# Optimization experiments

Hardware: AMD Instinct MI355X
Metric: run time of the kernel (lower is better)

Reference implementation:

```python
import jax, jax.numpy as jnp
import numpy as np

TOP_K = 2
AUX_COEF = 1e-3

def setup_inputs() -> dict:
    key = jax.random.key(0)
    ks = jax.random.split(key, 5)
    B, S, H, I, E = 4, 2048, 1024, 2048, 8
    x = jax.random.normal(ks[0], (B, S, H), jnp.float32)
    gate_w = jax.random.normal(ks[1], (H, E), jnp.float32) * 0.02
    w_gate = jax.random.normal(ks[2], (E, H, I), jnp.float32) * 0.02
    w_up = jax.random.normal(ks[3], (E, H, I), jnp.float32) * 0.02
    w_down = jax.random.normal(ks[4], (E, I, H), jnp.float32) * 0.02
    return {"x": x, "gate_w": gate_w, "w_gate": w_gate, "w_up": w_up, "w_down": w_down}


def reference(x, gate_w, w_gate, w_up, w_down):
    B, S, H = x.shape
    E = gate_w.shape[1]
    xf = x.reshape(-1, H)              # [N, H]
    N = xf.shape[0]

    # Router: softmax in fp32 (matches F.softmax(..., dtype=torch.float32))
    logits = xf @ gate_w               # [N, E]
    rw = jax.nn.softmax(logits.astype(jnp.float32), axis=-1).astype(x.dtype)
    top_w, top_i = jax.lax.top_k(rw, TOP_K)            # [N, K]
    top_w = top_w / top_w.sum(axis=-1, keepdims=True)  # renormalize

    # Combine weights: comb[t, e] = sum_k top_w[t,k] * (top_i[t,k]==e)
    comb = jnp.zeros((N, E), x.dtype).at[jnp.arange(N)[:, None], top_i].add(top_w)

    # SwiGLU FFN computed densely per expert, masked/combined by router weights
    h_gate = jax.nn.silu(jnp.einsum('th,ehi->eti', xf, w_gate))   # [E, N, I]
    h_up = jnp.einsum('th,ehi->eti', xf, w_up)                    # [E, N, I]
    expert_out = jnp.einsum('eti,eih->eth', h_gate * h_up, w_down)  # [E, N, H]
    y = jnp.einsum('eth,te->th', expert_out, comb).reshape(B, S, H)

    # Load-balancing aux loss
    sel_w = jnp.take_along_axis(rw, top_i, axis=1)   # router weight of chosen experts [N, K]
    load = jnp.zeros((E,), rw.dtype).at[top_i.reshape(-1)].add(sel_w.reshape(-1))
    P_expert = load / N
    counts = jnp.zeros((E,), jnp.float32).at[top_i.reshape(-1)].add(1.0)
    P_token_expert = counts / (N * TOP_K)
    aux_loss = (P_expert * P_token_expert).sum() * E * AUX_COEF
    return y, aux_loss
```

## Files before the change

kernel.cpp:

```cpp
#include <hip/hip_runtime.h>

#define N_TOK 8192
#define H_DIM 1024
#define I_DIM 2048
#define N_EXP 8
#define TOPK  2
#define CAP   17408
#define MT_MAX 136

#define OFF_TOPK_I 0u
#define OFF_TOPK_W 65536u
#define OFF_COUNTS 131072u
#define OFF_LOAD   131104u
#define OFF_CURSOR 131136u
#define OFF_PO     131168u
#define OFF_TILE_E 131232u
#define OFF_BTOK   131840u
#define OFF_BW     201472u
#define CTRL_BYTES 271104u
#define OFF_TSLOT  271104u
#define OFF_WGT  1048576u
#define OFF_WUT  (OFF_WGT + 33554432u)
#define OFF_WDT  (OFF_WUT + 33554432u)
#define OFF_HB   (OFF_WDT + 33554432u)
#define OFF_XB   (OFF_HB + 71303168u)

typedef __attribute__((ext_vector_type(8))) short bf16x8;
typedef __attribute__((ext_vector_type(8))) unsigned short u16x8;
typedef __attribute__((ext_vector_type(4))) unsigned short u16x4;
typedef __attribute__((ext_vector_type(4))) float f32x4;

__device__ __forceinline__ unsigned short f2bf(float f) {
  union { float f; unsigned int u; } v; v.f = f;
  unsigned int r = (v.u + 0x7FFFu + ((v.u >> 16) & 1u)) >> 16;
  return (unsigned short)r;
}
__device__ __forceinline__ float bf2f(unsigned short u) {
  union { unsigned int u; float f; } v; v.u = ((unsigned int)u) << 16;
  return v.f;
}
__device__ __forceinline__ u16x8 pack8(float4 a, float4 b) {
  u16x8 r;
  r[0] = f2bf(a.x); r[1] = f2bf(a.y); r[2] = f2bf(a.z); r[3] = f2bf(a.w);
  r[4] = f2bf(b.x); r[5] = f2bf(b.y); r[6] = f2bf(b.z); r[7] = f2bf(b.w);
  return r;
}
__device__ __forceinline__ f32x4 mfma32(bf16x8 a, bf16x8 b, f32x4 c) {
  return __builtin_amdgcn_mfma_f32_16x16x32_bf16(a, b, c, 0, 0, 0);
}
__device__ __forceinline__ void gll16(const void* g, void* l) {
  __builtin_amdgcn_global_load_lds(
      (const __attribute__((address_space(1))) unsigned int*)g,
      (__attribute__((address_space(3))) unsigned int*)l, 16, 0, 0);
}

__global__ __launch_bounds__(256) void k_xcast(const float* __restrict__ x,
                                               unsigned short* __restrict__ xb)
{
  int idx = blockIdx.x * 256 + threadIdx.x;
  const float4* s = (const float4*)x + (size_t)idx * 2;
  float4 a = s[0], b = s[1];
  *(u16x8*)&xb[(size_t)idx * 8] = pack8(a, b);
}

__global__ __launch_bounds__(256) void k_transpose(
    const float* __restrict__ wg, const float* __restrict__ wu, const float* __restrict__ wd,
    unsigned short* __restrict__ wgT, unsigned short* __restrict__ wuT,
    unsigned short* __restrict__ wdT)
{
  __shared__ unsigned short lds[64][65];
  int bid = blockIdx.x;
  int m = bid / 4096; int rem = bid % 4096;
  const float* src; unsigned short* dst; int R, C;
  if (m == 0)      { src = wg; dst = wgT; R = 1024; C = 2048; }
  else if (m == 1) { src = wu; dst = wuT; R = 1024; C = 2048; }
  else             { src = wd; dst = wdT; R = 2048; C = 1024; }
  int e = rem / 512; int trem = rem % 512;
  int tcc = C / 64;
  int r0 = (trem / tcc) * 64, c0 = (trem % tcc) * 64;
  size_t ebase = (size_t)e * R * C;
  dst += ebase;
  int tid = threadIdx.x;
  int lr = tid >> 3;
  int lc = (tid & 7) * 8;
#pragma unroll
  for (int p = 0; p < 2; ++p) {
    int row = p * 32 + lr;
    size_t off = ebase + (size_t)(r0 + row) * C + c0 + lc;
    float4 q0 = *(const float4*)&src[off];
    float4 q1 = *(const float4*)&src[off + 4];
    unsigned short tmp[8]; *(u16x8*)tmp = pack8(q0, q1);
#pragma unroll
    for (int j = 0; j < 8; ++j) lds[row][lc + j] = tmp[j];
  }
  __syncthreads();
#pragma unroll
  for (int p = 0; p < 2; ++p) {
    int drow = p * 32 + lr;
    unsigned short tmp[8];
#pragma unroll
    for (int j = 0; j < 8; ++j) tmp[j] = lds[lc + j][drow];
    *(u16x8*)&dst[(size_t)(c0 + drow) * R + r0 + lc] = *(const u16x8*)tmp;
  }
}

__global__ __launch_bounds__(256) void k_router(
    const float* __restrict__ x, const float* __restrict__ gw,
    int* __restrict__ topk_i, float* __restrict__ topk_w)
{
  int wave = threadIdx.x >> 6, lane = threadIdx.x & 63;
  int t = blockIdx.x * 4 + wave;
  const float* xr = x + (size_t)t * H_DIM;
  float acc[8];
#pragma unroll
  for (int e = 0; e < 8; ++e) acc[e] = 0.f;
#pragma unroll
  for (int it = 0; it < H_DIM / 64; ++it) {
    int h = it * 64 + lane;
    float xv = xr[h];
    float4 g0 = *(const float4*)&gw[h * 8];
    float4 g1 = *(const float4*)&gw[h * 8 + 4];
    acc[0] += xv * g0.x; acc[1] += xv * g0.y; acc[2] += xv * g0.z; acc[3] += xv * g0.w;
    acc[4] += xv * g1.x; acc[5] += xv * g1.y; acc[6] += xv * g1.z; acc[7] += xv * g1.w;
  }
#pragma unroll
  for (int off = 32; off > 0; off >>= 1) {
#pragma unroll
    for (int e = 0; e < 8; ++e) acc[e] += __shfl_xor(acc[e], off);
  }
  if (lane == 0) {
    float m = acc[0];
#pragma unroll
    for (int e = 1; e < 8; ++e) m = fmaxf(m, acc[e]);
    float p[8], s = 0.f;
#pragma unroll
    for (int e = 0; e < 8; ++e) { p[e] = __expf(acc[e] - m); s += p[e]; }
    float inv = 1.f / s;
#pragma unroll
    for (int e = 0; e < 8; ++e) p[e] *= inv;
    int i1 = 0;
#pragma unroll
    for (int e = 1; e < 8; ++e) if (p[e] > p[i1]) i1 = e;
    int i2 = (i1 == 0) ? 1 : 0;
#pragma unroll
    for (int e = 0; e < 8; ++e) if (e != i1 && p[e] > p[i2]) i2 = e;
    topk_i[t * 2]     = i1; topk_i[t * 2 + 1] = i2;
    topk_w[t * 2]     = p[i1]; topk_w[t * 2 + 1] = p[i2];
  }
}

__global__ __launch_bounds__(256) void k_hist(
    const int* __restrict__ topk_i, const float* __restrict__ topk_w,
    int* __restrict__ counts, float* __restrict__ loadw)
{
  __shared__ int c[8]; __shared__ float l[8];
  int tid = threadIdx.x;
  if (tid < 8) { c[tid] = 0; l[tid] = 0.f; }
  __syncthreads();
  int base = blockIdx.x * 1024 + tid * 4;
#pragma unroll
  for (int j = 0; j < 4; ++j) {
    int e = topk_i[base + j];
    float w = topk_w[base + j];
    atomicAdd(&c[e], 1);
    atomicAdd(&l[e], w);
  }
  __syncthreads();
  if (tid < 8) { atomicAdd(&counts[tid], c[tid]); atomicAdd(&loadw[tid], l[tid]); }
}

__global__ __launch_bounds__(256) void k_offsets(
    const int* __restrict__ counts, const float* __restrict__ loadw,
    int* __restrict__ po, int* __restrict__ tile_e, float* __restrict__ out)
{
  __shared__ int spo[9];
  if (threadIdx.x == 0) {
    int a = 0;
    for (int e = 0; e < 8; ++e) { spo[e] = a; po[e] = a; a += (counts[e] + 127) & ~127; }
    spo[8] = a; po[8] = a;
    float s = 0.f;
    for (int e = 0; e < 8; ++e) s += loadw[e] * (float)counts[e];
    out[(size_t)N_TOK * H_DIM] =
        s * ((float)N_EXP * 1e-3f) / ((float)N_TOK * (float)N_TOK * (float)TOPK);
  }
  __syncthreads();
  int mt = threadIdx.x;
  if (mt < MT_MAX) {
    int te = -1, beg = mt * 128;
    if (beg < spo[8]) {
      for (int e = 0; e < 8; ++e) if (beg >= spo[e] && beg < spo[e + 1]) te = e;
    }
    tile_e[mt] = te;
  }
}

__global__ __launch_bounds__(256) void k_bucket(
    const int* __restrict__ topk_i, const float* __restrict__ topk_w,
    const int* __restrict__ po, int* __restrict__ cursor,
    int* __restrict__ btok, float* __restrict__ bw, int* __restrict__ tslot)
{
  __shared__ int c[8];
  __shared__ int basee[8];
  int tid = threadIdx.x;
  if (tid < 8) c[tid] = 0;
  __syncthreads();
  int base = blockIdx.x * 1024 + tid * 4;
  int e4[4], r4[4]; float w4[4];
#pragma unroll
  for (int j = 0; j < 4; ++j) {
    int idx = base + j;
    int e = topk_i[idx];
    e4[j] = e;
    r4[j] = atomicAdd(&c[e], 1);
    int t = idx >> 1;
    float p0 = topk_w[t * 2], p1 = topk_w[t * 2 + 1];
    w4[j] = topk_w[idx] / (p0 + p1);
  }
  __syncthreads();
  if (tid < 8) basee[tid] = po[tid] + atomicAdd(&cursor[tid], c[tid]);
  __syncthreads();
#pragma unroll
  for (int j = 0; j < 4; ++j) {
    int idx = base + j;
    int slot = basee[e4[j]] + r4[j];
    btok[slot] = idx >> 1;
    bw[slot] = w4[j];
    tslot[idx] = slot;
  }
}

__global__ __launch_bounds__(256, 2) void k_gemm1(
    const unsigned short* __restrict__ xb,
    const unsigned short* __restrict__ wgT, const unsigned short* __restrict__ wuT,
    const int* __restrict__ btok, const int* __restrict__ tile_e,
    unsigned short* __restrict__ hbuf)
{
  int mt = blockIdx.y, nt = blockIdx.x;
  int e = tile_e[mt];
  if (e < 0) return;
  __shared__ unsigned short As[128 * 32];
  __shared__ unsigned short Bg[128 * 32];
  __shared__ unsigned short Bu[128 * 32];
  int tid = threadIdx.x;
  int wave = tid >> 6, lane = tid & 63;
  int wm = wave >> 1, wn = wave & 1;
  int quad = lane >> 4, l16 = lane & 15;

  int srow = lane >> 2;
  int sko  = (lane & 3) * 8;
  int ar0 = wave * 16 + srow;
  int ar1 = 64 + wave * 16 + srow;
  int t0 = btok[mt * 128 + ar0];
  int t1 = btok[mt * 128 + ar1];
  const unsigned short* ga0 = xb + (size_t)t0 * H_DIM + sko;
  const unsigned short* ga1 = xb + (size_t)t1 * H_DIM + sko;
  const unsigned short* bgb = wgT + ((size_t)e * I_DIM + nt * 128) * H_DIM;
  const unsigned short* bub = wuT + ((size_t)e * I_DIM + nt * 128) * H_DIM;
  const unsigned short* gg0 = bgb + (size_t)ar0 * H_DIM + sko;
  const unsigned short* gg1 = bgb + (size_t)ar1 * H_DIM + sko;
  const unsigned short* gu0 = bub + (size_t)ar0 * H_DIM + sko;
  const unsigned short* gu1 = bub + (size_t)ar1 * H_DIM + sko;
  unsigned lb0 = (unsigned)(wave * 16) * 32;
  unsigned lb1 = (unsigned)(64 + wave * 16) * 32;

  f32x4 accG[4][4], accU[4][4];
  f32x4 z = {0.f, 0.f, 0.f, 0.f};
#pragma unroll
  for (int i = 0; i < 4; ++i)
#pragma unroll
    for (int j = 0; j < 4; ++j) { accG[i][j] = z; accU[i][j] = z; }

  for (int k0 = 0; k0 < H_DIM; k0 += 32) {
    gll16(ga0 + k0, &As[lb0]);
    gll16(ga1 + k0, &As[lb1]);
    gll16(gg0 + k0, &Bg[lb0]);
    gll16(gg1 + k0, &Bg[lb1]);
    gll16(gu0 + k0, &Bu[lb0]);
    gll16(gu1 + k0, &Bu[lb1]);
    __syncthreads();
    bf16x8 af[4];
#pragma unroll
    for (int i = 0; i < 4; ++i)
      af[i] = *(const bf16x8*)&As[(wm * 64 + i * 16 + l16) * 32 + quad * 8];
#pragma unroll
    for (int j = 0; j < 4; ++j) {
      bf16x8 vg = *(const bf16x8*)&Bg[(wn * 64 + j * 16 + l16) * 32 + quad * 8];
      bf16x8 vu = *(const bf16x8*)&Bu[(wn * 64 + j * 16 + l16) * 32 + quad * 8];
#pragma unroll
      for (int i = 0; i < 4; ++i) {
        accG[i][j] = mfma32(af[i], vg, accG[i][j]);
        accU[i][j] = mfma32(af[i], vu, accU[i][j]);
      }
    }
    __syncthreads();
  }
#pragma unroll
  for (int i = 0; i < 4; ++i) {
#pragma unroll
    for (int r = 0; r < 4; ++r) {
      int row = mt * 128 + wm * 64 + i * 16 + quad * 4 + r;
      size_t base = (size_t)row * I_DIM + nt * 128 + wn * 64 + l16;
#pragma unroll
      for (int j = 0; j < 4; ++j) {
        float g = accG[i][j][r], u = accU[i][j][r];
        float sg = g / (1.f + __expf(-g));
        hbuf[base + j * 16] = f2bf(sg * u);
      }
    }
  }
}

__global__ __launch_bounds__(256, 2) void k_gemm2(
    const unsigned short* __restrict__ hbuf, const unsigned short* __restrict__ wdT,
    const int* __restrict__ tile_e, unsigned short* __restrict__ obuf)
{
  int mt = blockIdx.y, nt = blockIdx.x;
  int e = tile_e[mt];
  if (e < 0) return;
  __shared__ unsigned short As[128 * 32];
  __shared__ unsigned short Bs[128 * 32];
  int tid = threadIdx.x;
  int wave = tid >> 6, lane = tid & 63;
  int wm = wave >> 1, wn = wave & 1;
  int quad = lane >> 4, l16 = lane & 15;

  int srow = lane >> 2;
  int sko  = (lane & 3) * 8;
  int ar0 = wave * 16 + srow;
  int ar1 = 64 + wave * 16 + srow;
  const unsigned short* ga0 = hbuf + (size_t)(mt * 128 + ar0) * I_DIM + sko;
  const unsigned short* ga1 = hbuf + (size_t)(mt * 128 + ar1) * I_DIM + sko;
  const unsigned short* bb = wdT + ((size_t)e * H_DIM + nt * 128) * I_DIM;
  const unsigned short* gb0 = bb + (size_t)ar0 * I_DIM + sko;
  const unsigned short* gb1 = bb + (size_t)ar1 * I_DIM + sko;
  unsigned lb0 = (unsigned)(wave * 16) * 32;
  unsigned lb1 = (unsigned)(64 + wave * 16) * 32;

  f32x4 acc[4][4];
  f32x4 z = {0.f, 0.f, 0.f, 0.f};
#pragma unroll
  for (int i = 0; i < 4; ++i)
#pragma unroll
    for (int j = 0; j < 4; ++j) acc[i][j] = z;

  for (int k0 = 0; k0 < I_DIM; k0 += 32) {
    gll16(ga0 + k0, &As[lb0]);
    gll16(ga1 + k0, &As[lb1]);
    gll16(gb0 + k0, &Bs[lb0]);
    gll16(gb1 + k0, &Bs[lb1]);
    __syncthreads();
    bf16x8 af[4];
#pragma unroll
    for (int i = 0; i < 4; ++i)
      af[i] = *(const bf16x8*)&As[(wm * 64 + i * 16 + l16) * 32 + quad * 8];
#pragma unroll
    for (int j = 0; j < 4; ++j) {
      bf16x8 vb = *(const bf16x8*)&Bs[(wn * 64 + j * 16 + l16) * 32 + quad * 8];
#pragma unroll
      for (int i = 0; i < 4; ++i) acc[i][j] = mfma32(af[i], vb, acc[i][j]);
    }
    __syncthreads();
  }
#pragma unroll
  for (int i = 0; i < 4; ++i) {
#pragma unroll
    for (int r = 0; r < 4; ++r) {
      int s = mt * 128 + wm * 64 + i * 16 + quad * 4 + r;
      size_t base = (size_t)s * H_DIM + nt * 128 + wn * 64 + l16;
#pragma unroll
      for (int j = 0; j < 4; ++j)
        obuf[base + j * 16] = f2bf(acc[i][j][r]);
    }
  }
}

__global__ __launch_bounds__(256) void k_final(
    const unsigned short* __restrict__ obuf, const int* __restrict__ tslot,
    const float* __restrict__ bw, float* __restrict__ y)
{
  int t = blockIdx.x;
  int s0 = tslot[t * 2], s1 = tslot[t * 2 + 1];
  float w0 = bw[s0], w1 = bw[s1];
  int c = threadIdx.x * 4;
  u16x4 o0 = *(const u16x4*)&obuf[(size_t)s0 * H_DIM + c];
  u16x4 o1 = *(const u16x4*)&obuf[(size_t)s1 * H_DIM + c];
  float4 r;
  r.x = w0 * bf2f(o0[0]) + w1 * bf2f(o1[0]);
  r.y = w0 * bf2f(o0[1]) + w1 * bf2f(o1[1]);
  r.z = w0 * bf2f(o0[2]) + w1 * bf2f(o1[2]);
  r.w = w0 * bf2f(o0[3]) + w1 * bf2f(o1[3]);
  *(float4*)&y[(size_t)t * H_DIM + c] = r;
}

extern "C" void kernel_launch(void* const* d_in, const int* in_sizes, int n_in,
                              void* d_out, int out_size, void* d_ws, size_t ws_size,
                              hipStream_t stream)
{
  (void)in_sizes; (void)n_in; (void)out_size; (void)ws_size;
  const float* x  = (const float*)d_in[0];
  const float* gw = (const float*)d_in[1];
  const float* wg = (const float*)d_in[2];
  const float* wu = (const float*)d_in[3];
  const float* wd = (const float*)d_in[4];
  char* ws = (char*)d_ws;

  int*   topk_i = (int*)  (ws + OFF_TOPK_I);
  float* topk_w = (float*)(ws + OFF_TOPK_W);
  int*   counts = (int*)  (ws + OFF_COUNTS);
  float* loadw  = (float*)(ws + OFF_LOAD);
  int*   cursor = (int*)  (ws + OFF_CURSOR);
  int*   po     = (int*)  (ws + OFF_PO);
  int*   tile_e = (int*)  (ws + OFF_TILE_E);
  int*   btok   = (int*)  (ws + OFF_BTOK);
  float* bw     = (float*)(ws + OFF_BW);
  int*   tslot  = (int*)  (ws + OFF_TSLOT);
  unsigned short* wgT  = (unsigned short*)(ws + OFF_WGT);
  unsigned short* wuT  = (unsigned short*)(ws + OFF_WUT);
  unsigned short* wdT  = (unsigned short*)(ws + OFF_WDT);
  unsigned short* hbuf = (unsigned short*)(ws + OFF_HB);
  unsigned short* xb   = (unsigned short*)(ws + OFF_XB);
  unsigned short* obuf = (unsigned short*)(ws + OFF_WGT);
  float* yout = (float*)d_out;

  (void)hipMemsetAsync(ws, 0, CTRL_BYTES, stream);
  k_xcast<<<(N_TOK * H_DIM) / 2048, 256, 0, stream>>>(x, xb);
  k_transpose<<<12288, 256, 0, stream>>>(wg, wu, wd, wgT, wuT, wdT);
  k_router<<<N_TOK / 4, 256, 0, stream>>>(x, gw, topk_i, topk_w);
  k_hist<<<16, 256, 0, stream>>>(topk_i, topk_w, counts, loadw);
  k_offsets<<<1, 256, 0, stream>>>(counts, loadw, po, tile_e, (float*)d_out);
  k_bucket<<<16, 256, 0, stream>>>(topk_i, topk_w, po, cursor, btok, bw, tslot);
  k_gemm1<<<dim3(I_DIM / 128, MT_MAX), 256, 0, stream>>>(xb, wgT, wuT, btok, tile_e, hbuf);
  k_gemm2<<<dim3(H_DIM / 128, MT_MAX), 256, 0, stream>>>(hbuf, wdT, tile_e, obuf);
  k_final<<<N_TOK, 256, 0, stream>>>(obuf, tslot, bw, yout);
}
```

Before: 575.9 us.

## Rewrite expert GEMMs with 256-row tiles, swizzled LDS, multi-buffered prefetch pipelines

Both grouped GEMM kernels move to 512-thread blocks with 256-row M tiles, and expert buckets are padded to multiples of 256. The LDS layout uses a 64-wide K slab with an XOR swizzle to avoid bank conflicts. Global-to-LDS loads are prefetched into double buffers in gemm1 and triple buffers in gemm2, interleaved with MFMA phases using s_setprio and explicit vmcnt waits. The aim is to raise data reuse and hide memory latency, at the cost of more padding waste per expert and higher LDS use that limits occupancy.

```diff
diff --git a/kernel.cpp b/kernel.cpp
--- a/kernel.cpp
+++ b/kernel.cpp
@@ -5,8 +5,8 @@
 #define I_DIM 2048
 #define N_EXP 8
 #define TOPK  2
-#define CAP   17408
-#define MT_MAX 136
+#define CAP   18432
+#define MT_MAX 72
 
 #define OFF_TOPK_I 0u
 #define OFF_TOPK_W 65536u
@@ -15,20 +15,26 @@
 #define OFF_CURSOR 131136u
 #define OFF_PO     131168u
 #define OFF_TILE_E 131232u
-#define OFF_BTOK   131840u
-#define OFF_BW     201472u
-#define CTRL_BYTES 271104u
-#define OFF_TSLOT  271104u
+#define OFF_BTOK   131744u
+#define OFF_BW     205472u
+#define CTRL_BYTES 279200u
+#define OFF_TSLOT  279552u
 #define OFF_WGT  1048576u
 #define OFF_WUT  (OFF_WGT + 33554432u)
 #define OFF_WDT  (OFF_WUT + 33554432u)
 #define OFF_HB   (OFF_WDT + 33554432u)
-#define OFF_XB   (OFF_HB + 71303168u)
+#define OFF_XB   (OFF_HB + 75497472u)
 
 typedef __attribute__((ext_vector_type(8))) short bf16x8;
 typedef __attribute__((ext_vector_type(8))) unsigned short u16x8;
 typedef __attribute__((ext_vector_type(4))) unsigned short u16x4;
 typedef __attribute__((ext_vector_type(4))) float f32x4;
+
+#define BAR() __builtin_amdgcn_s_barrier()
+#define PRIO1() __builtin_amdgcn_s_setprio(1)
+#define PRIO0() __builtin_amdgcn_s_setprio(0)
+#define WAITV0() asm volatile("s_waitcnt vmcnt(0)" ::: "memory")
+#define WAITV6() asm volatile("s_waitcnt vmcnt(6)" ::: "memory")
 
 __device__ __forceinline__ unsigned short f2bf(float f) {
   union { float f; unsigned int u; } v; v.f = f;
@@ -176,7 +182,7 @@
   __shared__ int spo[9];
   if (threadIdx.x == 0) {
     int a = 0;
-    for (int e = 0; e < 8; ++e) { spo[e] = a; po[e] = a; a += (counts[e] + 127) & ~127; }
+    for (int e = 0; e < 8; ++e) { spo[e] = a; po[e] = a; a += (counts[e] + 255) & ~255; }
     spo[8] = a; po[8] = a;
     float s = 0.f;
     for (int e = 0; e < 8; ++e) s += loadw[e] * (float)counts[e];
@@ -186,7 +192,7 @@
   __syncthreads();
   int mt = threadIdx.x;
   if (mt < MT_MAX) {
-    int te = -1, beg = mt * 128;
+    int te = -1, beg = mt * 256;
     if (beg < spo[8]) {
       for (int e = 0; e < 8; ++e) if (beg >= spo[e] && beg < spo[e + 1]) te = e;
     }
@@ -229,7 +235,7 @@
   }
 }
 
-__global__ __launch_bounds__(256, 2) void k_gemm1(
+__global__ __launch_bounds__(512, 2) void k_gemm1(
     const unsigned short* __restrict__ xb,
     const unsigned short* __restrict__ wgT, const unsigned short* __restrict__ wuT,
     const int* __restrict__ btok, const int* __restrict__ tile_e,
@@ -238,30 +244,32 @@
   int mt = blockIdx.y, nt = blockIdx.x;
   int e = tile_e[mt];
   if (e < 0) return;
-  __shared__ unsigned short As[128 * 32];
-  __shared__ unsigned short Bg[128 * 32];
-  __shared__ unsigned short Bu[128 * 32];
+  __shared__ unsigned short lds[65536];
   int tid = threadIdx.x;
   int wave = tid >> 6, lane = tid & 63;
   int wm = wave >> 1, wn = wave & 1;
   int quad = lane >> 4, l16 = lane & 15;
 
-  int srow = lane >> 2;
-  int sko  = (lane & 3) * 8;
-  int ar0 = wave * 16 + srow;
-  int ar1 = 64 + wave * 16 + srow;
-  int t0 = btok[mt * 128 + ar0];
-  int t1 = btok[mt * 128 + ar1];
-  const unsigned short* ga0 = xb + (size_t)t0 * H_DIM + sko;
-  const unsigned short* ga1 = xb + (size_t)t1 * H_DIM + sko;
-  const unsigned short* bgb = wgT + ((size_t)e * I_DIM + nt * 128) * H_DIM;
-  const unsigned short* bub = wuT + ((size_t)e * I_DIM + nt * 128) * H_DIM;
-  const unsigned short* gg0 = bgb + (size_t)ar0 * H_DIM + sko;
-  const unsigned short* gg1 = bgb + (size_t)ar1 * H_DIM + sko;
-  const unsigned short* gu0 = bub + (size_t)ar0 * H_DIM + sko;
-  const unsigned short* gu1 = bub + (size_t)ar1 * H_DIM + sko;
-  unsigned lb0 = (unsigned)(wave * 16) * 32;
-  unsigned lb1 = (unsigned)(64 + wave * 16) * 32;
+  int rp = lane >> 3;
+  int chunk = (lane & 7) ^ rp;
+  const unsigned short* sA[2][2]; const unsigned short* sBg[2]; const unsigned short* sBu[2];
+  unsigned dA[2][2], dB[2];
+#pragma unroll
+  for (int h = 0; h < 2; ++h)
+#pragma unroll
+    for (int c = 0; c < 2; ++c) {
+      int rowp = wave * 16 + c * 8 + rp;
+      int tok = btok[mt * 256 + h * 128 + rowp];
+      sA[h][c] = xb + (size_t)tok * H_DIM + chunk * 8;
+      dA[h][c] = (unsigned)(h * 128 + wave * 16 + c * 8) * 64;
+    }
+#pragma unroll
+  for (int c = 0; c < 2; ++c) {
+    int rowp = wave * 16 + c * 8 + rp;
+    sBg[c] = wgT + ((size_t)e * I_DIM + nt * 128 + rowp) * H_DIM + chunk * 8;
+    sBu[c] = wuT + ((size_t)e * I_DIM + nt * 128 + rowp) * H_DIM + chunk * 8;
+    dB[c] = (unsigned)(wave * 16 + c * 8) * 64;
+  }
 
   f32x4 accG[4][4], accU[4][4];
   f32x4 z = {0.f, 0.f, 0.f, 0.f};
@@ -270,108 +278,251 @@
 #pragma unroll
     for (int j = 0; j < 4; ++j) { accG[i][j] = z; accU[i][j] = z; }
 
-  for (int k0 = 0; k0 < H_DIM; k0 += 32) {
-    gll16(ga0 + k0, &As[lb0]);
-    gll16(ga1 + k0, &As[lb1]);
-    gll16(gg0 + k0, &Bg[lb0]);
-    gll16(gg1 + k0, &Bg[lb1]);
-    gll16(gu0 + k0, &Bu[lb0]);
-    gll16(gu1 + k0, &Bu[lb1]);
-    __syncthreads();
-    bf16x8 af[4];
-#pragma unroll
-    for (int i = 0; i < 4; ++i)
-      af[i] = *(const bf16x8*)&As[(wm * 64 + i * 16 + l16) * 32 + quad * 8];
-#pragma unroll
-    for (int j = 0; j < 4; ++j) {
-      bf16x8 vg = *(const bf16x8*)&Bg[(wn * 64 + j * 16 + l16) * 32 + quad * 8];
-      bf16x8 vu = *(const bf16x8*)&Bu[(wn * 64 + j * 16 + l16) * 32 + quad * 8];
-#pragma unroll
-      for (int i = 0; i < 4; ++i) {
-        accG[i][j] = mfma32(af[i], vg, accG[i][j]);
-        accU[i][j] = mfma32(af[i], vu, accU[i][j]);
-      }
-    }
-    __syncthreads();
-  }
-#pragma unroll
-  for (int i = 0; i < 4; ++i) {
+  int fsw = l16 & 7;
+#pragma unroll
+  for (int h = 0; h < 2; ++h)
+#pragma unroll
+    for (int c = 0; c < 2; ++c) gll16(sA[h][c], &lds[dA[h][c]]);
+#pragma unroll
+  for (int c = 0; c < 2; ++c) { gll16(sBg[c], &lds[16384 + dB[c]]); gll16(sBu[c], &lds[24576 + dB[c]]); }
+  WAITV0();
+  BAR();
+
+  for (int t = 0; t < 16; ++t) {
+    unsigned bo = (unsigned)(t & 1) * 32768;
+    unsigned bo1 = bo ^ 32768;
+    int kel = (t + 1) * 64;
+    bool pf = (t < 15);
+    bf16x8 a[4][2];
+#pragma unroll
+    for (int m = 0; m < 4; ++m)
+#pragma unroll
+      for (int ks = 0; ks < 2; ++ks) {
+        int row = wm * 64 + m * 16 + l16;
+        a[m][ks] = *(const bf16x8*)&lds[bo + row * 64 + (((ks * 4 + quad) ^ fsw) * 8)];
+      }
+    bf16x8 bg[2][2];
+#pragma unroll
+    for (int nf = 0; nf < 2; ++nf)
+#pragma unroll
+      for (int ks = 0; ks < 2; ++ks) {
+        int col = wn * 64 + nf * 16 + l16;
+        bg[nf][ks] = *(const bf16x8*)&lds[bo + 16384 + col * 64 + (((ks * 4 + quad) ^ fsw) * 8)];
+      }
+    if (pf) {
+#pragma unroll
+      for (int h = 0; h < 2; ++h)
+#pragma unroll
+        for (int c = 0; c < 2; ++c) gll16(sA[h][c] + kel, &lds[bo1 + dA[h][c]]);
+    }
+    BAR();
+    PRIO1();
+#pragma unroll
+    for (int nf = 0; nf < 2; ++nf)
+#pragma unroll
+      for (int m = 0; m < 4; ++m)
+#pragma unroll
+        for (int ks = 0; ks < 2; ++ks) accG[m][nf] = mfma32(a[m][ks], bg[nf][ks], accG[m][nf]);
+    PRIO0();
+    BAR();
+#pragma unroll
+    for (int nf = 0; nf < 2; ++nf)
+#pragma unroll
+      for (int ks = 0; ks < 2; ++ks) {
+        int col = wn * 64 + (2 + nf) * 16 + l16;
+        bg[nf][ks] = *(const bf16x8*)&lds[bo + 16384 + col * 64 + (((ks * 4 + quad) ^ fsw) * 8)];
+      }
+    if (pf) {
+#pragma unroll
+      for (int c = 0; c < 2; ++c) { gll16(sBg[c] + kel, &lds[bo1 + 16384 + dB[c]]); gll16(sBu[c] + kel, &lds[bo1 + 24576 + dB[c]]); }
+    }
+    BAR();
+    PRIO1();
+#pragma unroll
+    for (int nf = 0; nf < 2; ++nf)
+#pragma unroll
+      for (int m = 0; m < 4; ++m)
+#pragma unroll
+        for (int ks = 0; ks < 2; ++ks) accG[m][2 + nf] = mfma32(a[m][ks], bg[nf][ks], accG[m][2 + nf]);
+    PRIO0();
+    BAR();
+#pragma unroll
+    for (int nf = 0; nf < 2; ++nf)
+#pragma unroll
+      for (int ks = 0; ks < 2; ++ks) {
+        int col = wn * 64 + nf * 16 + l16;
+        bg[nf][ks] = *(const bf16x8*)&lds[bo + 24576 + col * 64 + (((ks * 4 + quad) ^ fsw) * 8)];
+      }
+    BAR();
+    PRIO1();
+#pragma unroll
+    for (int nf = 0; nf < 2; ++nf)
+#pragma unroll
+      for (int m = 0; m < 4; ++m)
+#pragma unroll
+        for (int ks = 0; ks < 2; ++ks) accU[m][nf] = mfma32(a[m][ks], bg[nf][ks], accU[m][nf]);
+    PRIO0();
+    BAR();
+#pragma unroll
+    for (int nf = 0; nf < 2; ++nf)
+#pragma unroll
+      for (int ks = 0; ks < 2; ++ks) {
+        int col = wn * 64 + (2 + nf) * 16 + l16;
+        bg[nf][ks] = *(const bf16x8*)&lds[bo + 24576 + col * 64 + (((ks * 4 + quad) ^ fsw) * 8)];
+      }
+    BAR();
+    PRIO1();
+#pragma unroll
+    for (int nf = 0; nf < 2; ++nf)
+#pragma unroll
+      for (int m = 0; m < 4; ++m)
+#pragma unroll
+        for (int ks = 0; ks < 2; ++ks) accU[m][2 + nf] = mfma32(a[m][ks], bg[nf][ks], accU[m][2 + nf]);
+    PRIO0();
+    WAITV0();
+    BAR();
+  }
+#pragma unroll
+  for (int m = 0; m < 4; ++m)
 #pragma unroll
     for (int r = 0; r < 4; ++r) {
-      int row = mt * 128 + wm * 64 + i * 16 + quad * 4 + r;
+      int row = mt * 256 + wm * 64 + m * 16 + quad * 4 + r;
       size_t base = (size_t)row * I_DIM + nt * 128 + wn * 64 + l16;
 #pragma unroll
-      for (int j = 0; j < 4; ++j) {
-        float g = accG[i][j][r], u = accU[i][j][r];
+      for (int nf = 0; nf < 4; ++nf) {
+        float g = accG[m][nf][r], u = accU[m][nf][r];
         float sg = g / (1.f + __expf(-g));
-        hbuf[base + j * 16] = f2bf(sg * u);
-      }
-    }
-  }
-}
-
-__global__ __launch_bounds__(256, 2) void k_gemm2(
+        hbuf[base + nf * 16] = f2bf(sg * u);
+      }
+    }
+}
+
+__global__ __launch_bounds__(512, 2) void k_gemm2(
     const unsigned short* __restrict__ hbuf, const unsigned short* __restrict__ wdT,
     const int* __restrict__ tile_e, unsigned short* __restrict__ obuf)
 {
   int mt = blockIdx.y, nt = blockIdx.x;
   int e = tile_e[mt];
   if (e < 0) return;
-  __shared__ unsigned short As[128 * 32];
-  __shared__ unsigned short Bs[128 * 32];
+  __shared__ unsigned short lds[73728];
   int tid = threadIdx.x;
   int wave = tid >> 6, lane = tid & 63;
-  int wm = wave >> 1, wn = wave & 1;
+  int wm = wave >> 2, wn = wave & 3;
   int quad = lane >> 4, l16 = lane & 15;
 
-  int srow = lane >> 2;
-  int sko  = (lane & 3) * 8;
-  int ar0 = wave * 16 + srow;
-  int ar1 = 64 + wave * 16 + srow;
-  const unsigned short* ga0 = hbuf + (size_t)(mt * 128 + ar0) * I_DIM + sko;
-  const unsigned short* ga1 = hbuf + (size_t)(mt * 128 + ar1) * I_DIM + sko;
-  const unsigned short* bb = wdT + ((size_t)e * H_DIM + nt * 128) * I_DIM;
-  const unsigned short* gb0 = bb + (size_t)ar0 * I_DIM + sko;
-  const unsigned short* gb1 = bb + (size_t)ar1 * I_DIM + sko;
-  unsigned lb0 = (unsigned)(wave * 16) * 32;
-  unsigned lb1 = (unsigned)(64 + wave * 16) * 32;
-
-  f32x4 acc[4][4];
+  int rp = lane >> 3;
+  int chunk = (lane & 7) ^ rp;
+  const unsigned short* sA[2][2]; const unsigned short* sB[2];
+  unsigned dA[2][2], dB[2];
+#pragma unroll
+  for (int h = 0; h < 2; ++h)
+#pragma unroll
+    for (int c = 0; c < 2; ++c) {
+      int rowp = wave * 16 + c * 8 + rp;
+      sA[h][c] = hbuf + (size_t)(mt * 256 + h * 128 + rowp) * I_DIM + chunk * 8;
+      dA[h][c] = (unsigned)(h * 128 + wave * 16 + c * 8) * 64;
+    }
+#pragma unroll
+  for (int c = 0; c < 2; ++c) {
+    int rowp = wave * 16 + c * 8 + rp;
+    sB[c] = wdT + ((size_t)e * H_DIM + nt * 128 + rowp) * I_DIM + chunk * 8;
+    dB[c] = (unsigned)(wave * 16 + c * 8) * 64;
+  }
+
+  f32x4 acc[8][2];
   f32x4 z = {0.f, 0.f, 0.f, 0.f};
 #pragma unroll
-  for (int i = 0; i < 4; ++i)
-#pragma unroll
-    for (int j = 0; j < 4; ++j) acc[i][j] = z;
-
-  for (int k0 = 0; k0 < I_DIM; k0 += 32) {
-    gll16(ga0 + k0, &As[lb0]);
-    gll16(ga1 + k0, &As[lb1]);
-    gll16(gb0 + k0, &Bs[lb0]);
-    gll16(gb1 + k0, &Bs[lb1]);
-    __syncthreads();
-    bf16x8 af[4];
-#pragma unroll
-    for (int i = 0; i < 4; ++i)
-      af[i] = *(const bf16x8*)&As[(wm * 64 + i * 16 + l16) * 32 + quad * 8];
-#pragma unroll
-    for (int j = 0; j < 4; ++j) {
-      bf16x8 vb = *(const bf16x8*)&Bs[(wn * 64 + j * 16 + l16) * 32 + quad * 8];
-#pragma unroll
-      for (int i = 0; i < 4; ++i) acc[i][j] = mfma32(af[i], vb, acc[i][j]);
-    }
-    __syncthreads();
-  }
-#pragma unroll
-  for (int i = 0; i < 4; ++i) {
+  for (int i = 0; i < 8; ++i) { acc[i][0] = z; acc[i][1] = z; }
+
+  int fsw = l16 & 7;
+#pragma unroll
+  for (int tt = 0; tt < 2; ++tt) {
+    unsigned bo = (unsigned)tt * 24576;
+    int kel = tt * 64;
+#pragma unroll
+    for (int h = 0; h < 2; ++h)
+#pragma unroll
+      for (int c = 0; c < 2; ++c) gll16(sA[h][c] + kel, &lds[bo + dA[h][c]]);
+#pragma unroll
+    for (int c = 0; c < 2; ++c) gll16(sB[c] + kel, &lds[bo + 16384 + dB[c]]);
+  }
+  WAITV6();
+  BAR();
+
+  unsigned boA = 0, boB = 24576, boC = 49152;
+  for (int t = 0; t < 32; ++t) {
+    int kel = (t + 2) * 64;
+    bool pf = (t < 30);
+    bf16x8 b[2][2];
+#pragma unroll
+    for (int nf = 0; nf < 2; ++nf)
+#pragma unroll
+      for (int ks = 0; ks < 2; ++ks) {
+        int col = wn * 32 + nf * 16 + l16;
+        b[nf][ks] = *(const bf16x8*)&lds[boA + 16384 + col * 64 + (((ks * 4 + quad) ^ fsw) * 8)];
+      }
+    {
+      bf16x8 a[4][2];
+#pragma unroll
+      for (int m = 0; m < 4; ++m)
+#pragma unroll
+        for (int ks = 0; ks < 2; ++ks) {
+          int row = wm * 128 + m * 16 + l16;
+          a[m][ks] = *(const bf16x8*)&lds[boA + row * 64 + (((ks * 4 + quad) ^ fsw) * 8)];
+        }
+      if (pf) {
+#pragma unroll
+        for (int h = 0; h < 2; ++h)
+#pragma unroll
+          for (int c = 0; c < 2; ++c) gll16(sA[h][c] + kel, &lds[boC + dA[h][c]]);
+      }
+      BAR();
+      PRIO1();
+#pragma unroll
+      for (int m = 0; m < 4; ++m)
+#pragma unroll
+        for (int nf = 0; nf < 2; ++nf)
+#pragma unroll
+          for (int ks = 0; ks < 2; ++ks) acc[m][nf] = mfma32(a[m][ks], b[nf][ks], acc[m][nf]);
+      PRIO0();
+      BAR();
+    }
+    {
+      bf16x8 a[4][2];
+#pragma unroll
+      for (int m = 0; m < 4; ++m)
+#pragma unroll
+        for (int ks = 0; ks < 2; ++ks) {
+          int row = wm * 128 + (4 + m) * 16 + l16;
+          a[m][ks] = *(const bf16x8*)&lds[boA + row * 64 + (((ks * 4 + quad) ^ fsw) * 8)];
+        }
+      if (pf) {
+#pragma unroll
+        for (int c = 0; c < 2; ++c) gll16(sB[c] + kel, &lds[boC + 16384 + dB[c]]);
+      }
+      BAR();
+      PRIO1();
+#pragma unroll
+      for (int m = 0; m < 4; ++m)
+#pragma unroll
+        for (int nf = 0; nf < 2; ++nf)
+#pragma unroll
+          for (int ks = 0; ks < 2; ++ks) acc[4 + m][nf] = mfma32(a[m][ks], b[nf][ks], acc[4 + m][nf]);
+      PRIO0();
+    }
+    if (pf) { WAITV6(); } else { WAITV0(); }
+    BAR();
+    unsigned tmp = boA; boA = boB; boB = boC; boC = tmp;
+  }
+#pragma unroll
+  for (int m = 0; m < 8; ++m)
 #pragma unroll
     for (int r = 0; r < 4; ++r) {
-      int s = mt * 128 + wm * 64 + i * 16 + quad * 4 + r;
-      size_t base = (size_t)s * H_DIM + nt * 128 + wn * 64 + l16;
-#pragma unroll
-      for (int j = 0; j < 4; ++j)
-        obuf[base + j * 16] = f2bf(acc[i][j][r]);
-    }
-  }
+      int s = mt * 256 + wm * 128 + m * 16 + quad * 4 + r;
+      size_t base = (size_t)s * H_DIM + nt * 128 + wn * 32 + l16;
+      obuf[base]      = f2bf(acc[m][0][r]);
+      obuf[base + 16] = f2bf(acc[m][1][r]);
+    }
 }
 
 __global__ __launch_bounds__(256) void k_final(
@@ -429,7 +580,7 @@
   k_hist<<<16, 256, 0, stream>>>(topk_i, topk_w, counts, loadw);
   k_offsets<<<1, 256, 0, stream>>>(counts, loadw, po, tile_e, (float*)d_out);
   k_bucket<<<16, 256, 0, stream>>>(topk_i, topk_w, po, cursor, btok, bw, tslot);
-  k_gemm1<<<dim3(I_DIM / 128, MT_MAX), 256, 0, stream>>>(xb, wgT, wuT, btok, tile_e, hbuf);
-  k_gemm2<<<dim3(H_DIM / 128, MT_MAX), 256, 0, stream>>>(hbuf, wdT, tile_e, obuf);
+  k_gemm1<<<dim3(I_DIM / 128, MT_MAX), 512, 0, stream>>>(xb, wgT, wuT, btok, tile_e, hbuf);
+  k_gemm2<<<dim3(H_DIM / 128, MT_MAX), 512, 0, stream>>>(hbuf, wdT, tile_e, obuf);
   k_final<<<N_TOK, 256, 0, stream>>>(obuf, tslot, bw, yout);
 }
```

Result: faster. 561.0 us (-2.6%).
